# Kernel tuning notes

Hardware: AMD Instinct MI355X
Metric: run time of the kernel (lower is better)

## Reference

```python
import jax, jax.numpy as jnp
import numpy as np

L, H, NH, HD, F, B, S = 32, 1024, 16, 64, 2048, 2, 2048
HPH = H // NH  # hidden per attention head (hyena column split)
EPS = 1e-6
BLOCK = {0:'HCS',4:'HCS',7:'HCS',11:'HCS',14:'HCS',18:'HCS',21:'HCS',25:'HCS',28:'HCS',
         1:'HCM',5:'HCM',8:'HCM',12:'HCM',15:'HCM',19:'HCM',22:'HCM',26:'HCM',29:'HCM',
         2:'HCL',6:'HCL',9:'HCL',13:'HCL',16:'HCL',20:'HCL',23:'HCL',27:'HCL',30:'HCL',
         3:'ATT',10:'ATT',17:'ATT',24:'ATT',31:'ATT'}

def rmsnorm(x, w):
    return x * jax.lax.rsqrt(jnp.mean(x * x, -1, keepdims=True) + EPS) * w

def step_fir(u, state, w, b, flip=False, gated=False):
    # u:[B,C]  state:[B,C,cache]  w:[C,Lf]  b:[C]  (single-token FIR step)
    cache = state.shape[-1]
    w = w[:, ::-1][:, -(cache + 1):] if flip else w[:, :cache + 1]
    y = w[:, -1] * u + jnp.sum(state * w[:, :-1], -1)
    y = y + (b * u if gated else b)
    return y

def split3(z):
    # column_split_hyena=True path of _interleave_split
    r = z.reshape(z.shape[0], NH, 3 * HPH)
    x2 = r[:, :, :HPH].reshape(z.shape[0], H)
    x1 = r[:, :, HPH:2 * HPH].reshape(z.shape[0], H)
    v = r[:, :, 2 * HPH:].reshape(z.shape[0], H)
    return x2, x1, v

def mlp(x, W1, W2):
    return jax.nn.gelu(x @ W1.T) @ W2.T

def fir_block(x, n1, n2, pW, pb, oW, ob, W1, W2, sfw, sfb, h, D, fstate, istate, flip, gated):
    xn = rmsnorm(x, n1)
    z = xn @ pW.T + pb                 # [B,1,3H]
    u = z[:, -1]                       # [B,3H]
    zp = step_fir(u, fstate, sfw, sfb)
    x2, x1, v = split3(zp)
    y = step_fir(x1 * v, istate, h, D, flip=flip, gated=gated)
    y = (y * x2)[:, None]              # [B,1,H]
    x = y @ oW.T + ob + x
    return mlp(rmsnorm(x, n2), W1, W2) + x

def hcl_block(x, n1, n2, pW, pb, oW, ob, W1, W2, sfw, sfb, log_poles, residues, D, fstate, iir):
    xn = rmsnorm(x, n1)
    z = xn @ pW.T + pb
    u = z[:, -1]
    zp = step_fir(u, fstate, sfw, sfb)
    x2, x1, v = split3(zp)
    x1v = x1 * v
    iir_new = jnp.exp(log_poles) * iir + x1v[..., None]   # [B,H,SS] single-step IIR update
    res = jnp.sum(residues * iir_new, -1)
    y = (x2 * (res + D * x1v))[:, None]
    x = y @ oW.T + ob + x
    return mlp(rmsnorm(x, n2), W1, W2) + x

def att_block(x, n1, n2, qW, qb, oW, ob, W1, W2, kc, vc, cos, sin, pos):
    xn = rmsnorm(x, n1)
    qkv = (xn @ qW.T + qb).reshape(B, 1, 3, NH, HD)
    q, k, v = qkv[:, :, 0], qkv[:, :, 1], qkv[:, :, 2]
    c = jnp.concatenate([cos[pos], cos[pos]])  # [HD]
    s = jnp.concatenate([sin[pos], sin[pos]])
    rot = lambda t: jnp.concatenate([-t[..., HD // 2:], t[..., :HD // 2]], -1)
    q = q * c + rot(q) * s
    k = k * c + rot(k) * s
    kc = kc.at[:, pos].set(k[:, 0])  # KV-cache scatter write at current position
    vc = vc.at[:, pos].set(v[:, 0])
    scores = jnp.einsum('bohd,bshd->bhos', q, kc) * (HD ** -0.5)
    scores = jnp.where(jnp.arange(S) > pos, -10000.0, scores)
    aw = jax.nn.softmax(scores, -1)
    ctx = jnp.einsum('bhos,bshd->bohd', aw, vc).reshape(B, 1, H)
    x = ctx @ oW.T + ob + x
    return mlp(rmsnorm(x, n2), W1, W2) + x

def forward(x, position, norm1_w, norm2_w, proj_W, proj_b, out_W, out_b, mlp_W1, mlp_W2,
            sf_w, sf_b, hcs_h, hcs_D, hcm_h, hcm_D, hcl_logpoles, hcl_residues, hcl_D,
            fir_state, hcs_state, hcm_state, iir_state, k_cache, v_cache, rope_cos, rope_sin):
    att = 0
    for i in range(L):  # loop over 32 structurally distinct layers (static)
        t = BLOCK[i]
        cm = (norm1_w[i], norm2_w[i], proj_W[i], proj_b[i], out_W[i], out_b[i], mlp_W1[i], mlp_W2[i])
        if t == 'HCS':
            x = fir_block(x, *cm, sf_w[i], sf_b[i], hcs_h[i], hcs_D[i], fir_state[i], hcs_state[i], False, False)
        elif t == 'HCM':
            x = fir_block(x, *cm, sf_w[i], sf_b[i], hcm_h[i], hcm_D[i], fir_state[i], hcm_state[i], True, True)
        elif t == 'HCL':
            x = hcl_block(x, *cm, sf_w[i], sf_b[i], hcl_logpoles[i], hcl_residues[i], hcl_D[i], fir_state[i], iir_state[i])
        else:
            x = att_block(x, *cm, k_cache[att], v_cache[att], rope_cos, rope_sin, position)
            att += 1
    return x

def setup_inputs():
    key = jax.random.key(0)
    ks = jax.random.split(key, 24)
    g = lambda k, shape, sc: jax.random.normal(k, shape, jnp.float32) * sc
    inv_freq = 1.0 / (10000.0 ** (np.arange(0, HD, 2, dtype=np.float32) / HD))
    ang = np.arange(S, dtype=np.float32)[:, None] * inv_freq[None, :]
    return {
        'x': g(ks[0], (B, 1, H), 1.0),
        'position': 1024,
        'norm1_w': jnp.ones((L, H), jnp.float32),
        'norm2_w': jnp.ones((L, H), jnp.float32),
        'proj_W': g(ks[1], (L, 3 * H, H), H ** -0.5),
        'proj_b': jnp.zeros((L, 3 * H), jnp.float32),
        'out_W': g(ks[2], (L, H, H), 0.2 * H ** -0.5),
        'out_b': jnp.zeros((L, H), jnp.float32),
        'mlp_W1': g(ks[3], (L, F, H), H ** -0.5),
        'mlp_W2': g(ks[4], (L, H, F), 0.2 * F ** -0.5),
        'sf_w': g(ks[5], (L, 3 * H, 3), 0.4),
        'sf_b': g(ks[6], (L, 3 * H), 0.02),
        'hcs_h': g(ks[7], (L, H, 7), 0.2),
        'hcs_D': g(ks[8], (L, H), 0.2),
        'hcm_h': g(ks[9], (L, H, 128), 0.04),
        'hcm_D': g(ks[10], (L, H), 0.2),
        'hcl_logpoles': -jax.random.uniform(ks[11], (L, H, 16), jnp.float32, 0.01, 2.0),
        'hcl_residues': g(ks[12], (L, H, 16), 0.1),
        'hcl_D': g(ks[13], (L, H), 0.2),
        'fir_state': g(ks[14], (L, B, 3 * H, 2), 0.5),
        'hcs_state': g(ks[15], (L, B, H, 6), 0.5),
        'hcm_state': g(ks[16], (L, B, H, 127), 0.5),
        'iir_state': g(ks[17], (L, B, H, 16), 0.5),
        'k_cache': g(ks[18], (5, B, S, NH, HD), 1.0),
        'v_cache': g(ks[19], (5, B, S, NH, HD), 1.0),
        'rope_cos': jnp.asarray(np.cos(ang)),
        'rope_sin': jnp.asarray(np.sin(ang)),
    }

def reference(x, position, norm1_w, norm2_w, proj_W, proj_b, out_W, out_b, mlp_W1, mlp_W2,
              sf_w, sf_b, hcs_h, hcs_D, hcm_h, hcm_D, hcl_logpoles, hcl_residues, hcl_D,
              fir_state, hcs_state, hcm_state, iir_state, k_cache, v_cache, rope_cos, rope_sin):
    return forward(x, position, norm1_w, norm2_w, proj_W, proj_b, out_W, out_b, mlp_W1, mlp_W2,
                   sf_w, sf_b, hcs_h, hcs_D, hcm_h, hcm_D, hcl_logpoles, hcl_residues, hcl_D,
                   fir_state, hcs_state, hcm_state, iir_state, k_cache, v_cache, rope_cos, rope_sin)
```

## Files before the change

kernel.cpp:

```cpp
#include <hip/hip_runtime.h>
#include <hip/hip_bf16.h>
#include <math.h>

#define LAYERS 32
#define H      1024
#define H3     3072
#define NHEADS 16
#define HDIM   64
#define FF     2048
#define BATCH  2
#define SEQ    2048
#define EPSF   1e-6f

__device__ __forceinline__ float wredSum(float v) {
#pragma unroll
  for (int m = 32; m >= 1; m >>= 1) v += __shfl_xor(v, m, 64);
  return v;
}
__device__ __forceinline__ float wredMax(float v) {
#pragma unroll
  for (int m = 32; m >= 1; m >>= 1) v = fmaxf(v, __shfl_xor(v, m, 64));
  return v;
}
__device__ __forceinline__ float gelu_t(float x) {
  return 0.5f * x * (1.0f + tanhf(0.7978845608028654f * (x + 0.044715f * x * x * x)));
}
__device__ __forceinline__ float dot4(float4 a, float4 b) {
  return a.x * b.x + a.y * b.y + a.z * b.z + a.w * b.w;
}

__global__ __launch_bounds__(256) void prep_kernel(
    const float* __restrict__ sf_w, const float* __restrict__ sf_b,
    const float* __restrict__ fir_state,
    const float* __restrict__ hcs_h, const float* __restrict__ hcs_D, const float* __restrict__ hcs_state,
    const float* __restrict__ hcm_h, const float* __restrict__ hcm_D, const float* __restrict__ hcm_state,
    const float* __restrict__ lp, const float* __restrict__ resd, const float* __restrict__ hcl_D,
    const float* __restrict__ iir,
    unsigned long long kbits,
    float* __restrict__ sfd, float* __restrict__ sfc,
    float* __restrict__ mix0, float* __restrict__ mix1)
{
  int blk = blockIdx.x, tid = threadIdx.x;
  if (blk < 768) {
    int idx = blk * 256 + tid;
    int i = idx / (BATCH * H3);
    int r = idx % (BATCH * H3);
    int b = r / H3, ch = r % H3;
    const float* fs = fir_state + ((size_t)(i * BATCH + b) * H3 + ch) * 2;
    const float* sw = sf_w + ((size_t)i * H3 + ch) * 3;
    sfd[idx] = fs[0] * sw[0] + fs[1] * sw[1] + sf_b[i * H3 + ch];
    if (b == 0) sfc[i * H3 + ch] = sw[2];
  } else if (blk < 1024) {
    int idx = (blk - 768) * 256 + tid;
    int i = idx >> 11;
    int r = idx & 2047;
    int b = r >> 10, c = r & 1023;
    int kind = (int)((kbits >> (2 * i)) & 3ull);
    if (kind == 0) {
      const float* st = hcs_state + ((size_t)(i * BATCH + b) * H + c) * 6;
      const float* hh = hcs_h + ((size_t)i * H + c) * 7;
      float acc = 0.f;
#pragma unroll
      for (int k = 0; k < 6; k++) acc += st[k] * hh[k];
      mix0[idx] = acc + hcs_D[i * H + c];
      if (b == 0) mix1[i * H + c] = hh[6];
    } else if (kind == 2) {
      const float* ii = iir + ((size_t)(i * BATCH + b) * H + c) * 16;
      const float* lpp = lp + ((size_t)i * H + c) * 16;
      const float* rs = resd + ((size_t)i * H + c) * 16;
      float acc = 0.f, rsum = 0.f;
#pragma unroll
      for (int k = 0; k < 16; k++) { float rv = rs[k]; acc += rv * expf(lpp[k]) * ii[k]; rsum += rv; }
      mix0[idx] = acc;
      if (b == 0) mix1[i * H + c] = rsum + hcl_D[i * H + c];
    }
  } else {
    int w = tid >> 6, lane = tid & 63;
    int widx = (blk - 1024) * 4 + w;
    if (widx < 9 * BATCH * H) {
      int li = widx >> 11;
      int r = widx & 2047;
      int b = r >> 10, c = r & 1023;
      int i = (li >> 1) * 7 + ((li & 1) ? 5 : 1);
      const float* st = hcm_state + ((size_t)(i * BATCH + b) * H + c) * 127;
      const float* hh = hcm_h + ((size_t)i * H + c) * 128;
      float acc = 0.f;
      int k = lane;
      if (k < 127) acc += st[k] * hh[127 - k];
      k = lane + 64;
      if (k < 127) acc += st[k] * hh[127 - k];
      acc = wredSum(acc);
      if (lane == 0) {
        mix0[(i * BATCH + b) * H + c] = acc;
        if (b == 0) mix1[i * H + c] = hh[0] + hcm_D[i * H + c];
      }
    }
  }
}

template<int ROWS, bool GELU, bool HASBIAS>
__global__ __launch_bounds__(256) void gemv_norm(
    const float* __restrict__ x, const float* __restrict__ nw,
    const float* __restrict__ W, const float* __restrict__ bias,
    float* __restrict__ out)
{
  __shared__ alignas(16) float xe[BATCH * H];
  __shared__ float red[8];
  int tid = threadIdx.x, lane = tid & 63, w = tid >> 6;

  float4 xv0 = ((const float4*)x)[tid];
  float4 xv1 = ((const float4*)x)[tid + 256];
  float4 nv  = ((const float4*)nw)[tid];
  int r = blockIdx.x * 4 + w;
  const float4* rowp = (const float4*)(W + (size_t)r * H);
  float4 wv0 = rowp[lane], wv1 = rowp[lane + 64],
         wv2 = rowp[lane + 128], wv3 = rowp[lane + 192];

  float ss0 = dot4(xv0, xv0), ss1 = dot4(xv1, xv1);
  ((float4*)xe)[tid]       = make_float4(xv0.x * nv.x, xv0.y * nv.y, xv0.z * nv.z, xv0.w * nv.w);
  ((float4*)xe)[tid + 256] = make_float4(xv1.x * nv.x, xv1.y * nv.y, xv1.z * nv.z, xv1.w * nv.w);
  ss0 = wredSum(ss0); ss1 = wredSum(ss1);
  if (lane == 0) { red[w] = ss0; red[4 + w] = ss1; }
  __syncthreads();
  float s0 = rsqrtf((red[0] + red[1] + red[2] + red[3]) * (1.0f / H) + EPSF);
  float s1 = rsqrtf((red[4] + red[5] + red[6] + red[7]) * (1.0f / H) + EPSF);

  const float4* x4 = (const float4*)xe;
  float a0 = dot4(wv0, x4[lane])       + dot4(wv1, x4[lane + 64])
           + dot4(wv2, x4[lane + 128]) + dot4(wv3, x4[lane + 192]);
  float a1 = dot4(wv0, x4[lane + 256]) + dot4(wv1, x4[lane + 320])
           + dot4(wv2, x4[lane + 384]) + dot4(wv3, x4[lane + 448]);
  a0 = wredSum(a0); a1 = wredSum(a1);
  if (lane == 0) {
    float b0 = HASBIAS ? bias[r] : 0.f;
    float v0 = a0 * s0 + b0, v1 = a1 * s1 + b0;
    if (GELU) { v0 = gelu_t(v0); v1 = gelu_t(v1); }
    out[r] = v0;
    out[ROWS + r] = v1;
  }
}

__global__ __launch_bounds__(256) void mix_out_kernel(
    int kind,
    const float* __restrict__ z, const float* __restrict__ sfdL, const float* __restrict__ sfcL,
    const float* __restrict__ mix0L, const float* __restrict__ mix1L,
    const float* __restrict__ attP,
    const float* __restrict__ oW, const float* __restrict__ ob,
    const float* __restrict__ x_in, float* __restrict__ x_out)
{
  __shared__ alignas(16) float ys[BATCH * H];
  int tid = threadIdx.x, lane = tid & 63, w = tid >> 6;
  int r = blockIdx.x * 4 + w;

  if (kind < 3) {
    float x2v[8], x1v[8], vvv[8];
#pragma unroll
    for (int it = 0; it < 8; it++) {
      int e = tid + it * 256;
      int b = e >> 10, c = e & 1023;
      int n = c >> 6, d = c & 63;
      int base = n * 192 + d;
      x2v[it] = sfcL[base] * z[b * H3 + base] + sfdL[b * H3 + base];
      x1v[it] = sfcL[base + 64] * z[b * H3 + base + 64] + sfdL[b * H3 + base + 64];
      vvv[it] = sfcL[base + 128] * z[b * H3 + base + 128] + sfdL[b * H3 + base + 128];
    }
    const float4* rowp = (const float4*)(oW + (size_t)r * H);
    float4 wv0 = rowp[lane], wv1 = rowp[lane + 64],
           wv2 = rowp[lane + 128], wv3 = rowp[lane + 192];
#pragma unroll
    for (int it = 0; it < 8; it++) {
      int e = tid + it * 256;
      int b = e >> 10, c = e & 1023;
      float t = x1v[it] * vvv[it];
      ys[e] = (mix1L[c] * t + mix0L[b * H + c]) * x2v[it];
    }
    __syncthreads();
    const float4* y4 = (const float4*)ys;
    float a0 = dot4(wv0, y4[lane])       + dot4(wv1, y4[lane + 64])
             + dot4(wv2, y4[lane + 128]) + dot4(wv3, y4[lane + 192]);
    float a1 = dot4(wv0, y4[lane + 256]) + dot4(wv1, y4[lane + 320])
             + dot4(wv2, y4[lane + 384]) + dot4(wv3, y4[lane + 448]);
    a0 = wredSum(a0); a1 = wredSum(a1);
    if (lane == 0) {
      x_out[r]     = a0 + ob[r] + x_in[r];
      x_out[H + r] = a1 + ob[r] + x_in[H + r];
    }
  } else {
    const float4* rowp = (const float4*)(oW + (size_t)r * H);
    float4 wv0 = rowp[lane], wv1 = rowp[lane + 64],
           wv2 = rowp[lane + 128], wv3 = rowp[lane + 192];
#pragma unroll
    for (int it = 0; it < 8; it++) {
      int e = tid + it * 256;
      int b = e >> 10, c = e & 1023;
      int n = c >> 6, d = c & 63;
      float M = -1e30f;
#pragma unroll
      for (int sp = 0; sp < 8; sp++) M = fmaxf(M, attP[((sp * BATCH + b) * NHEADS + n) * 66 + 64]);
      float Ls = 0.f, num = 0.f;
#pragma unroll
      for (int sp = 0; sp < 8; sp++) {
        const float* P = attP + ((sp * BATCH + b) * NHEADS + n) * 66;
        float wgt = expf(P[64] - M);
        Ls += wgt * P[65];
        num += wgt * P[d];
      }
      ys[e] = num / Ls;
    }
    __syncthreads();
    const float4* y4 = (const float4*)ys;
    float a0 = dot4(wv0, y4[lane])       + dot4(wv1, y4[lane + 64])
             + dot4(wv2, y4[lane + 128]) + dot4(wv3, y4[lane + 192]);
    float a1 = dot4(wv0, y4[lane + 256]) + dot4(wv1, y4[lane + 320])
             + dot4(wv2, y4[lane + 384]) + dot4(wv3, y4[lane + 448]);
    a0 = wredSum(a0); a1 = wredSum(a1);
    if (lane == 0) {
      x_out[r]     = a0 + ob[r] + x_in[r];
      x_out[H + r] = a1 + ob[r] + x_in[H + r];
    }
  }
}

__global__ __launch_bounds__(256) void gemv_mlp2(
    const float* __restrict__ h, const float* __restrict__ W2,
    const float* __restrict__ xM, float* __restrict__ x_out)
{
  __shared__ alignas(16) float hs[BATCH * FF];
  int tid = threadIdx.x, lane = tid & 63, w = tid >> 6;
  float4 h0 = ((const float4*)h)[tid];
  float4 h1 = ((const float4*)h)[tid + 256];
  float4 h2 = ((const float4*)h)[tid + 512];
  float4 h3 = ((const float4*)h)[tid + 768];
  int r = blockIdx.x * 4 + w;
  const float4* rowp = (const float4*)(W2 + (size_t)r * FF);
  float4 wv[8];
#pragma unroll
  for (int j = 0; j < 8; j++) wv[j] = rowp[lane + 64 * j];

  ((float4*)hs)[tid]       = h0;
  ((float4*)hs)[tid + 256] = h1;
  ((float4*)hs)[tid + 512] = h2;
  ((float4*)hs)[tid + 768] = h3;
  __syncthreads();

  const float4* h4 = (const float4*)hs;
  float a0 = 0.f, a1 = 0.f;
#pragma unroll
  for (int j = 0; j < 8; j++) {
    a0 += dot4(wv[j], h4[lane + 64 * j]);
    a1 += dot4(wv[j], h4[lane + 64 * j + 512]);
  }
  a0 = wredSum(a0); a1 = wredSum(a1);
  if (lane == 0) {
    x_out[r]     = a0 + xM[r];
    x_out[H + r] = a1 + xM[H + r];
  }
}

__global__ __launch_bounds__(256) void attn_kernel(
    const float* __restrict__ z, const int* __restrict__ posp,
    const float* __restrict__ kc, const float* __restrict__ vc,
    const float* __restrict__ cosT, const float* __restrict__ sinT,
    float* __restrict__ P)
{
  int sp = blockIdx.x & 7, n = (blockIdx.x >> 3) & 15, b = blockIdx.x >> 7;
  int pos = *posp;
  __shared__ alignas(16) float q_s[HDIM], k_s[HDIM], v_s[HDIM];
  __shared__ float eg[256];
  __shared__ float redA[4];
  __shared__ alignas(16) float osum[4][HDIM];
  int tid = threadIdx.x, lane = tid & 63, w = tid >> 6;

  if (tid < 64) {
    int d = tid, j = d & 31;
    float cs = cosT[pos * 32 + j], sn = sinT[pos * 32 + j];
    float qv = z[b * H3 + n * 64 + d];
    float qo = z[b * H3 + n * 64 + ((d + 32) & 63)];
    q_s[d] = ((d < 32) ? (qv * cs - qo * sn) : (qv * cs + qo * sn)) * 0.125f;
    float kv = z[b * H3 + 1024 + n * 64 + d];
    float ko = z[b * H3 + 1024 + n * 64 + ((d + 32) & 63)];
    k_s[d] = (d < 32) ? (kv * cs - ko * sn) : (kv * cs + ko * sn);
    v_s[d] = z[b * H3 + 2048 + n * 64 + d];
  }
  __syncthreads();

  int s = sp * 256 + tid;
  float logit = -1e30f;
  if (s <= pos) {
    const float4* k4 = (s == pos) ? (const float4*)k_s
                                  : (const float4*)(kc + (((size_t)b * SEQ + s) * NHEADS + n) * HDIM);
    const float4* q4 = (const float4*)q_s;
    float acc = 0.f;
#pragma unroll
    for (int j = 0; j < 16; j++) acc += dot4(k4[j], q4[j]);
    logit = acc;
  }
  float m = wredMax(logit);
  if (lane == 0) redA[w] = m;
  __syncthreads();
  m = fmaxf(fmaxf(redA[0], redA[1]), fmaxf(redA[2], redA[3]));
  float e = (s <= pos) ? expf(logit - m) : 0.f;
  eg[tid] = e;
  float ps = wredSum(e);
  __syncthreads();
  if (lane == 0) redA[w] = ps;
  __syncthreads();
  float lsum = redA[0] + redA[1] + redA[2] + redA[3];

  int dgrp = lane & 15, srow = lane >> 4;
  float4 acc = make_float4(0.f, 0.f, 0.f, 0.f);
#pragma unroll 4
  for (int it = 0; it < 16; it++) {
    int sl = w * 64 + it * 4;
    if (sp * 256 + sl > pos) break;
    int sli = sl + srow;
    int ss = sp * 256 + sli;
    float ev = eg[sli];
    const float4* v4 = (ss == pos) ? (const float4*)v_s
                                   : (const float4*)(vc + (((size_t)b * SEQ + ss) * NHEADS + n) * HDIM);
    float4 vv = v4[dgrp];
    acc.x += ev * vv.x; acc.y += ev * vv.y; acc.z += ev * vv.z; acc.w += ev * vv.w;
  }
#pragma unroll
  for (int mm = 16; mm <= 32; mm <<= 1) {
    acc.x += __shfl_xor(acc.x, mm, 64);
    acc.y += __shfl_xor(acc.y, mm, 64);
    acc.z += __shfl_xor(acc.z, mm, 64);
    acc.w += __shfl_xor(acc.w, mm, 64);
  }
  if (srow == 0) ((float4*)osum[w])[dgrp] = acc;
  __syncthreads();
  float* Pp = P + ((size_t)(sp * BATCH + b) * NHEADS + n) * 66;
  if (tid < 64) Pp[tid] = osum[0][tid] + osum[1][tid] + osum[2][tid] + osum[3][tid];
  if (tid == 64) Pp[64] = m;
  if (tid == 65) Pp[65] = lsum;
}

extern "C" void kernel_launch(void* const* d_in, const int* in_sizes, int n_in,
                              void* d_out, int out_size, void* d_ws, size_t ws_size,
                              hipStream_t stream) {
  (void)in_sizes; (void)n_in; (void)out_size; (void)ws_size;
  const float* x0    = (const float*)d_in[0];
  const int*   posp  = (const int*)d_in[1];
  const float* n1    = (const float*)d_in[2];
  const float* n2    = (const float*)d_in[3];
  const float* pW    = (const float*)d_in[4];
  const float* pb    = (const float*)d_in[5];
  const float* oW    = (const float*)d_in[6];
  const float* ob    = (const float*)d_in[7];
  const float* W1    = (const float*)d_in[8];
  const float* W2    = (const float*)d_in[9];
  const float* sfw   = (const float*)d_in[10];
  const float* sfb   = (const float*)d_in[11];
  const float* hcs_h = (const float*)d_in[12];
  const float* hcs_D = (const float*)d_in[13];
  const float* hcm_h = (const float*)d_in[14];
  const float* hcm_D = (const float*)d_in[15];
  const float* lp    = (const float*)d_in[16];
  const float* resd  = (const float*)d_in[17];
  const float* hclD  = (const float*)d_in[18];
  const float* fir   = (const float*)d_in[19];
  const float* hcsS  = (const float*)d_in[20];
  const float* hcmS  = (const float*)d_in[21];
  const float* iir   = (const float*)d_in[22];
  const float* kc    = (const float*)d_in[23];
  const float* vc    = (const float*)d_in[24];
  const float* cosT  = (const float*)d_in[25];
  const float* sinT  = (const float*)d_in[26];

  float* ws    = (float*)d_ws;
  float* xbuf0 = ws;
  float* xbuf1 = ws + 2048;
  float* xM    = ws + 4096;
  float* zbuf  = ws + 6144;
  float* hbuf  = ws + 12288;
  float* attP  = ws + 16384;
  float* sfd   = ws + 33280;
  float* sfc   = ws + 229888;
  float* mix0  = ws + 328192;
  float* mix1  = ws + 393728;

  static const int KIND[LAYERS] = {0,1,2,3,0,1,2,0,1,2,3,0,1,2,0,1,2,3,0,1,2,0,1,2,3,0,1,2,0,1,2,3};
  unsigned long long kbits = 0ull;
  for (int i = 0; i < LAYERS; i++) kbits |= ((unsigned long long)KIND[i]) << (2 * i);

  prep_kernel<<<5632, 256, 0, stream>>>(sfw, sfb, fir, hcs_h, hcs_D, hcsS,
      hcm_h, hcm_D, hcmS, lp, resd, hclD, iir, kbits, sfd, sfc, mix0, mix1);

  const float* xsrc = x0;
  int att = 0;
  for (int i = 0; i < LAYERS; i++) {
    gemv_norm<H3, false, true><<<H3 / 4, 256, 0, stream>>>(
        xsrc, n1 + i * H, pW + (size_t)i * H3 * H, pb + i * H3, zbuf);
    if (KIND[i] == 3) {
      attn_kernel<<<256, 256, 0, stream>>>(
          zbuf, posp, kc + (size_t)att * BATCH * SEQ * NHEADS * HDIM,
          vc + (size_t)att * BATCH * SEQ * NHEADS * HDIM, cosT, sinT, attP);
      att++;
    }
    mix_out_kernel<<<H / 4, 256, 0, stream>>>(
        KIND[i], zbuf, sfd + (size_t)i * BATCH * H3, sfc + (size_t)i * H3,
        mix0 + (size_t)i * BATCH * H, mix1 + (size_t)i * H, attP,
        oW + (size_t)i * H * H, ob + i * H, xsrc, xM);
    gemv_norm<FF, true, false><<<FF / 4, 256, 0, stream>>>(
        xM, n2 + i * H, W1 + (size_t)i * FF * H, nullptr, hbuf);
    float* xout = (i == LAYERS - 1) ? (float*)d_out : ((i & 1) ? xbuf1 : xbuf0);
    gemv_mlp2<<<H / 4, 256, 0, stream>>>(
        hbuf, W2 + (size_t)i * H * FF, xM, xout);
    xsrc = xout;
  }
}
```

Measured before the change: 681.1 us.

## Prefetch upcoming layer weights and KV cache into L2 via extra blocks

Adds extra thread blocks to each kernel launch that read ahead the weights needed by later kernels (oW and W1 during the projection GEMV, W2 and the next layer's pW during mix_out and MLP1) and the next attention layer's KV cache during MLP2. The reads are summed and discarded, so they serve only to warm the cache. This aims to hide the DRAM latency of the weight-streaming GEMV chain, which is memory bound at batch 2. In exchange it adds redundant memory traffic and competes for bandwidth and CUs with the real work, and it relies on the prefetched data still being resident in L2/MALL when it is used.

```diff
diff --git a/kernel.cpp b/kernel.cpp
--- a/kernel.cpp
+++ b/kernel.cpp
@@ -29,6 +29,20 @@
   return a.x * b.x + a.y * b.y + a.z * b.z + a.w * b.w;
 }
 
+__device__ __forceinline__ void pf_region(const float4* __restrict__ p, long long n4, int chunk) {
+  long long base = (long long)chunk * 4096 + threadIdx.x;
+  float a0 = 0.f, a1 = 0.f, a2 = 0.f, a3 = 0.f;
+#pragma unroll
+  for (int j = 0; j < 16; j++) {
+    long long idx = base + j * 256;
+    if (idx < n4) {
+      float4 v = p[idx];
+      a0 += v.x; a1 += v.y; a2 += v.z; a3 += v.w;
+    }
+  }
+  asm volatile("" :: "v"(a0), "v"(a1), "v"(a2), "v"(a3));
+}
+
 __global__ __launch_bounds__(256) void prep_kernel(
     const float* __restrict__ sf_w, const float* __restrict__ sf_b,
     const float* __restrict__ fir_state,
@@ -38,9 +52,11 @@
     const float* __restrict__ iir,
     unsigned long long kbits,
     float* __restrict__ sfd, float* __restrict__ sfc,
-    float* __restrict__ mix0, float* __restrict__ mix1)
+    float* __restrict__ mix0, float* __restrict__ mix1,
+    const float4* __restrict__ pf0)
 {
   int blk = blockIdx.x, tid = threadIdx.x;
+  if (blk >= 5632) { pf_region(pf0, 786432LL, blk - 5632); return; }
   if (blk < 768) {
     int idx = blk * 256 + tid;
     int i = idx / (BATCH * H3);
@@ -102,11 +118,20 @@
 __global__ __launch_bounds__(256) void gemv_norm(
     const float* __restrict__ x, const float* __restrict__ nw,
     const float* __restrict__ W, const float* __restrict__ bias,
-    float* __restrict__ out)
+    float* __restrict__ out,
+    const float4* __restrict__ pf0, int c0, long long n0,
+    const float4* __restrict__ pf1, int c1, long long n1)
 {
   __shared__ alignas(16) float xe[BATCH * H];
   __shared__ float red[8];
   int tid = threadIdx.x, lane = tid & 63, w = tid >> 6;
+  const int NFUNC = ROWS / 4;
+  if (blockIdx.x >= NFUNC) {
+    int c = blockIdx.x - NFUNC;
+    if (c < c0) pf_region(pf0, n0, c);
+    else pf_region(pf1, n1, c - c0);
+    return;
+  }
 
   float4 xv0 = ((const float4*)x)[tid];
   float4 xv1 = ((const float4*)x)[tid + 256];
@@ -146,10 +171,18 @@
     const float* __restrict__ mix0L, const float* __restrict__ mix1L,
     const float* __restrict__ attP,
     const float* __restrict__ oW, const float* __restrict__ ob,
-    const float* __restrict__ x_in, float* __restrict__ x_out)
+    const float* __restrict__ x_in, float* __restrict__ x_out,
+    const float4* __restrict__ pf0, int c0, long long n0,
+    const float4* __restrict__ pf1, int c1, long long n1)
 {
   __shared__ alignas(16) float ys[BATCH * H];
   int tid = threadIdx.x, lane = tid & 63, w = tid >> 6;
+  if (blockIdx.x >= 256) {
+    int c = blockIdx.x - 256;
+    if (c < c0) pf_region(pf0, n0, c);
+    else pf_region(pf1, n1, c - c0);
+    return;
+  }
   int r = blockIdx.x * 4 + w;
 
   if (kind < 3) {
@@ -223,10 +256,21 @@
 
 __global__ __launch_bounds__(256) void gemv_mlp2(
     const float* __restrict__ h, const float* __restrict__ W2,
-    const float* __restrict__ xM, float* __restrict__ x_out)
+    const float* __restrict__ xM, float* __restrict__ x_out,
+    const float* __restrict__ kvk, const float* __restrict__ kvv,
+    const int* __restrict__ posp)
 {
   __shared__ alignas(16) float hs[BATCH * FF];
   int tid = threadIdx.x, lane = tid & 63, w = tid >> 6;
+  if (blockIdx.x >= 256) {
+    int c = blockIdx.x - 256;
+    int reg = c >> 7, ch = c & 127;
+    const float* base = (reg & 1) ? kvv : kvk;
+    base += (size_t)(reg >> 1) * SEQ * NHEADS * HDIM;
+    long long n4 = ((long long)(posp[0] + 1) * NHEADS * HDIM) >> 2;
+    pf_region((const float4*)base, n4, ch);
+    return;
+  }
   float4 h0 = ((const float4*)h)[tid];
   float4 h1 = ((const float4*)h)[tid + 256];
   float4 h2 = ((const float4*)h)[tid + 512];
@@ -384,29 +428,43 @@
   unsigned long long kbits = 0ull;
   for (int i = 0; i < LAYERS; i++) kbits |= ((unsigned long long)KIND[i]) << (2 * i);
 
-  prep_kernel<<<5632, 256, 0, stream>>>(sfw, sfb, fir, hcs_h, hcs_D, hcsS,
-      hcm_h, hcm_D, hcmS, lp, resd, hclD, iir, kbits, sfd, sfc, mix0, mix1);
+  prep_kernel<<<5632 + 192, 256, 0, stream>>>(sfw, sfb, fir, hcs_h, hcs_D, hcsS,
+      hcm_h, hcm_D, hcmS, lp, resd, hclD, iir, kbits, sfd, sfc, mix0, mix1,
+      (const float4*)pW);
 
   const float* xsrc = x0;
   int att = 0;
   for (int i = 0; i < LAYERS; i++) {
-    gemv_norm<H3, false, true><<<H3 / 4, 256, 0, stream>>>(
-        xsrc, n1 + i * H, pW + (size_t)i * H3 * H, pb + i * H3, zbuf);
+    gemv_norm<H3, false, true><<<768 + 192, 256, 0, stream>>>(
+        xsrc, n1 + i * H, pW + (size_t)i * H3 * H, pb + i * H3, zbuf,
+        (const float4*)(oW + (size_t)i * H * H), 64, 262144LL,
+        (const float4*)(W1 + (size_t)i * FF * H), 128, 524288LL);
     if (KIND[i] == 3) {
       attn_kernel<<<256, 256, 0, stream>>>(
           zbuf, posp, kc + (size_t)att * BATCH * SEQ * NHEADS * HDIM,
           vc + (size_t)att * BATCH * SEQ * NHEADS * HDIM, cosT, sinT, attP);
       att++;
     }
-    mix_out_kernel<<<H / 4, 256, 0, stream>>>(
+    int cmix = (i < 31) ? 96 : 0;
+    mix_out_kernel<<<256 + 128 + cmix, 256, 0, stream>>>(
         KIND[i], zbuf, sfd + (size_t)i * BATCH * H3, sfc + (size_t)i * H3,
         mix0 + (size_t)i * BATCH * H, mix1 + (size_t)i * H, attP,
-        oW + (size_t)i * H * H, ob + i * H, xsrc, xM);
-    gemv_norm<FF, true, false><<<FF / 4, 256, 0, stream>>>(
-        xM, n2 + i * H, W1 + (size_t)i * FF * H, nullptr, hbuf);
+        oW + (size_t)i * H * H, ob + i * H, xsrc, xM,
+        (const float4*)(W2 + (size_t)i * H * FF), 128, 524288LL,
+        (i < 31) ? (const float4*)(pW + (size_t)(i + 1) * H3 * H) : (const float4*)pW,
+        cmix, 393216LL);
+    int cw1 = (i < 31) ? 96 : 0;
+    gemv_norm<FF, true, false><<<512 + cw1, 256, 0, stream>>>(
+        xM, n2 + i * H, W1 + (size_t)i * FF * H, nullptr, hbuf,
+        (i < 31) ? (const float4*)(pW + (size_t)(i + 1) * H3 * H + 1572864) : (const float4*)pW,
+        cw1, 393216LL,
+        (const float4*)pW, 0, 0LL);
+    bool nextAtt = (i < 31) && (KIND[i + 1] == 3);
+    const float* kcn = nextAtt ? (kc + (size_t)att * BATCH * SEQ * NHEADS * HDIM) : kc;
+    const float* vcn = nextAtt ? (vc + (size_t)att * BATCH * SEQ * NHEADS * HDIM) : vc;
     float* xout = (i == LAYERS - 1) ? (float*)d_out : ((i & 1) ? xbuf1 : xbuf0);
-    gemv_mlp2<<<H / 4, 256, 0, stream>>>(
-        hbuf, W2 + (size_t)i * H * FF, xM, xout);
+    gemv_mlp2<<<256 + (nextAtt ? 512 : 0), 256, 0, stream>>>(
+        hbuf, W2 + (size_t)i * H * FF, xM, xout, kcn, vcn, posp);
     xsrc = xout;
   }
 }
```

Result: slower. 1.204 ms (+76.7%).

## Fuse each layer's GEMV stages into one kernel with atomic-counter dataflow sync

Applied to the files above, without the earlier changes.

Replaces the per-layer sequence of separate launches (input projection, attention, output mix, MLP up, MLP down) with a single kernel per layer. Each stage gets its own block range. Each block loads its weight rows before spinning on global atomic counters that track the previous stage's progress. This removes launch gaps and kernel-boundary drains and lets weight streaming for later stages overlap with earlier compute. The barrier counters are zeroed in the prep kernel. It relies on in-order block dispatch and relaxed atomics for forward progress and visibility, which risks deadlock or stale reads if producer blocks are not resident.

```diff
diff --git a/kernel.cpp b/kernel.cpp
--- a/kernel.cpp
+++ b/kernel.cpp
@@ -17,6 +17,11 @@
   for (int m = 32; m >= 1; m >>= 1) v += __shfl_xor(v, m, 64);
   return v;
 }
+__device__ __forceinline__ int iwredSum(int v) {
+#pragma unroll
+  for (int m = 32; m >= 1; m >>= 1) v += __shfl_xor(v, m, 64);
+  return v;
+}
 __device__ __forceinline__ float wredMax(float v) {
 #pragma unroll
   for (int m = 32; m >= 1; m >>= 1) v = fmaxf(v, __shfl_xor(v, m, 64));
@@ -27,6 +32,295 @@
 }
 __device__ __forceinline__ float dot4(float4 a, float4 b) {
   return a.x * b.x + a.y * b.y + a.z * b.z + a.w * b.w;
+}
+
+__device__ __forceinline__ void ast(float* p, float v) {
+  __hip_atomic_store(p, v, __ATOMIC_RELAXED, __HIP_MEMORY_SCOPE_AGENT);
+}
+__device__ __forceinline__ float ald(const float* p) {
+  return __hip_atomic_load(p, __ATOMIC_RELAXED, __HIP_MEMORY_SCOPE_AGENT);
+}
+
+__device__ __forceinline__ void signal_grp(int* grp, int bid) {
+  __syncthreads();
+  if (threadIdx.x == 0)
+    __hip_atomic_fetch_add(&grp[(bid & 63) * 16], 1, __ATOMIC_RELAXED, __HIP_MEMORY_SCOPE_AGENT);
+}
+__device__ __forceinline__ void wait_grp(int* grp, int need) {
+  if (threadIdx.x < 64) {
+    for (;;) {
+      int v = __hip_atomic_load(&grp[threadIdx.x * 16], __ATOMIC_RELAXED, __HIP_MEMORY_SCOPE_AGENT);
+      if (iwredSum(v) >= need) break;
+      __builtin_amdgcn_s_sleep(2);
+    }
+  }
+  __syncthreads();
+  asm volatile("" ::: "memory");
+}
+
+union SH2 {
+  struct { float xe[2048]; float red[8]; } ns;
+  struct { float ys[2048]; float sml[512]; } mx;
+  struct { float hs[4096]; } w2;
+  struct { float q[64]; float k[64]; float v[64]; float eg[256]; float redA[4]; float osum[4][64]; } att;
+};
+
+__global__ __launch_bounds__(256, 6) void layer_k(
+    int kind,
+    const float* __restrict__ xin, float* __restrict__ xout,
+    const float* __restrict__ n1L, const float* __restrict__ n2L,
+    const float* __restrict__ pWL, const float* __restrict__ pbL,
+    const float* __restrict__ oWL, const float* __restrict__ obL,
+    const float* __restrict__ W1L, const float* __restrict__ W2L,
+    const float* __restrict__ sfcL, const float* __restrict__ sfdL,
+    const float* __restrict__ mix0L, const float* __restrict__ mix1L,
+    const float* __restrict__ kcL, const float* __restrict__ vcL,
+    const int* __restrict__ posp,
+    const float* __restrict__ cosT, const float* __restrict__ sinT,
+    float* __restrict__ z, float* __restrict__ attP,
+    float* __restrict__ xM, float* __restrict__ h,
+    int* __restrict__ barL)
+{
+  __shared__ SH2 sh;
+  int bid = blockIdx.x, tid = threadIdx.x, lane = tid & 63, w = tid >> 6;
+  int* cnt0 = barL;
+  int* cnt1 = barL + 1024;
+  int* cnt2 = barL + 2048;
+  int* cnt3 = barL + 3072;
+
+  int mixBase = (kind == 3) ? 1024 : 768;
+  int w1Base  = (kind == 3) ? 1280 : 1024;
+  int w2Base  = w1Base + 512;
+
+  if (bid < 768) {
+    float4 xv0 = ((const float4*)xin)[tid];
+    float4 xv1 = ((const float4*)xin)[tid + 256];
+    float4 nv  = ((const float4*)n1L)[tid];
+    int r = bid * 4 + w;
+    const float4* rowp = (const float4*)(pWL + (size_t)r * H);
+    float4 wv0 = rowp[lane], wv1 = rowp[lane + 64],
+           wv2 = rowp[lane + 128], wv3 = rowp[lane + 192];
+
+    float ss0 = dot4(xv0, xv0), ss1 = dot4(xv1, xv1);
+    ((float4*)sh.ns.xe)[tid]       = make_float4(xv0.x * nv.x, xv0.y * nv.y, xv0.z * nv.z, xv0.w * nv.w);
+    ((float4*)sh.ns.xe)[tid + 256] = make_float4(xv1.x * nv.x, xv1.y * nv.y, xv1.z * nv.z, xv1.w * nv.w);
+    ss0 = wredSum(ss0); ss1 = wredSum(ss1);
+    if (lane == 0) { sh.ns.red[w] = ss0; sh.ns.red[4 + w] = ss1; }
+    __syncthreads();
+    float s0 = rsqrtf((sh.ns.red[0] + sh.ns.red[1] + sh.ns.red[2] + sh.ns.red[3]) * (1.0f / H) + EPSF);
+    float s1 = rsqrtf((sh.ns.red[4] + sh.ns.red[5] + sh.ns.red[6] + sh.ns.red[7]) * (1.0f / H) + EPSF);
+
+    const float4* x4 = (const float4*)sh.ns.xe;
+    float a0 = dot4(wv0, x4[lane])       + dot4(wv1, x4[lane + 64])
+             + dot4(wv2, x4[lane + 128]) + dot4(wv3, x4[lane + 192]);
+    float a1 = dot4(wv0, x4[lane + 256]) + dot4(wv1, x4[lane + 320])
+             + dot4(wv2, x4[lane + 384]) + dot4(wv3, x4[lane + 448]);
+    a0 = wredSum(a0); a1 = wredSum(a1);
+    if (lane == 0) {
+      float b0 = pbL[r];
+      ast(&z[r], a0 * s0 + b0);
+      ast(&z[H3 + r], a1 * s1 + b0);
+    }
+    signal_grp(cnt0, bid);
+
+  } else if (kind == 3 && bid < 1024) {
+    int mb = bid - 768;
+    int sp = mb & 7, n = (mb >> 3) & 15, b = mb >> 7;
+    int pos = *posp;
+    wait_grp(cnt0, 768);
+    if (tid < 64) {
+      int d = tid, j = d & 31;
+      float cs = cosT[pos * 32 + j], sn = sinT[pos * 32 + j];
+      float qv = ald(&z[b * H3 + n * 64 + d]);
+      float qo = ald(&z[b * H3 + n * 64 + ((d + 32) & 63)]);
+      sh.att.q[d] = ((d < 32) ? (qv * cs - qo * sn) : (qv * cs + qo * sn)) * 0.125f;
+      float kv = ald(&z[b * H3 + 1024 + n * 64 + d]);
+      float ko = ald(&z[b * H3 + 1024 + n * 64 + ((d + 32) & 63)]);
+      sh.att.k[d] = (d < 32) ? (kv * cs - ko * sn) : (kv * cs + ko * sn);
+      sh.att.v[d] = ald(&z[b * H3 + 2048 + n * 64 + d]);
+    }
+    __syncthreads();
+    int s = sp * 256 + tid;
+    float logit = -1e30f;
+    if (s <= pos) {
+      const float4* k4 = (s == pos) ? (const float4*)sh.att.k
+                                    : (const float4*)(kcL + (((size_t)b * SEQ + s) * NHEADS + n) * HDIM);
+      const float4* q4 = (const float4*)sh.att.q;
+      float acc = 0.f;
+#pragma unroll
+      for (int j = 0; j < 16; j++) acc += dot4(k4[j], q4[j]);
+      logit = acc;
+    }
+    float m = wredMax(logit);
+    if (lane == 0) sh.att.redA[w] = m;
+    __syncthreads();
+    m = fmaxf(fmaxf(sh.att.redA[0], sh.att.redA[1]), fmaxf(sh.att.redA[2], sh.att.redA[3]));
+    float e = (s <= pos) ? expf(logit - m) : 0.f;
+    sh.att.eg[tid] = e;
+    float ps = wredSum(e);
+    __syncthreads();
+    if (lane == 0) sh.att.redA[w] = ps;
+    __syncthreads();
+    float lsum = sh.att.redA[0] + sh.att.redA[1] + sh.att.redA[2] + sh.att.redA[3];
+
+    int dgrp = lane & 15, srow = lane >> 4;
+    float4 acc = make_float4(0.f, 0.f, 0.f, 0.f);
+#pragma unroll 4
+    for (int it = 0; it < 16; it++) {
+      int sl = w * 64 + it * 4;
+      if (sp * 256 + sl > pos) break;
+      int sli = sl + srow;
+      int ss2 = sp * 256 + sli;
+      float ev = sh.att.eg[sli];
+      const float4* v4 = (ss2 == pos) ? (const float4*)sh.att.v
+                                      : (const float4*)(vcL + (((size_t)b * SEQ + ss2) * NHEADS + n) * HDIM);
+      float4 vv = v4[dgrp];
+      acc.x += ev * vv.x; acc.y += ev * vv.y; acc.z += ev * vv.z; acc.w += ev * vv.w;
+    }
+#pragma unroll
+    for (int mm = 16; mm <= 32; mm <<= 1) {
+      acc.x += __shfl_xor(acc.x, mm, 64);
+      acc.y += __shfl_xor(acc.y, mm, 64);
+      acc.z += __shfl_xor(acc.z, mm, 64);
+      acc.w += __shfl_xor(acc.w, mm, 64);
+    }
+    if (srow == 0) ((float4*)sh.att.osum[w])[dgrp] = acc;
+    __syncthreads();
+    float* Pp = attP + (size_t)((sp * BATCH + b) * NHEADS + n) * 66;
+    if (tid < 64) ast(&Pp[tid], sh.att.osum[0][tid] + sh.att.osum[1][tid] + sh.att.osum[2][tid] + sh.att.osum[3][tid]);
+    if (tid == 64) ast(&Pp[64], m);
+    if (tid == 65) ast(&Pp[65], lsum);
+    signal_grp(cnt1, bid);
+
+  } else if (bid < w1Base) {
+    int mb = bid - mixBase;
+    int r = mb * 4 + w;
+    const float4* rowp = (const float4*)(oWL + (size_t)r * H);
+    float4 wv0 = rowp[lane], wv1 = rowp[lane + 64],
+           wv2 = rowp[lane + 128], wv3 = rowp[lane + 192];
+
+    if (kind != 3) {
+      wait_grp(cnt0, 768);
+#pragma unroll
+      for (int it = 0; it < 8; it++) {
+        int e = tid + it * 256;
+        int b = e >> 10, c = e & 1023;
+        int n = c >> 6, d = c & 63;
+        int base = n * 192 + d;
+        float z0 = ald(&z[b * H3 + base]);
+        float z1 = ald(&z[b * H3 + base + 64]);
+        float z2 = ald(&z[b * H3 + base + 128]);
+        float x2 = sfcL[base] * z0 + sfdL[b * H3 + base];
+        float x1 = sfcL[base + 64] * z1 + sfdL[b * H3 + base + 64];
+        float vv = sfcL[base + 128] * z2 + sfdL[b * H3 + base + 128];
+        float t = x1 * vv;
+        sh.mx.ys[e] = (mix1L[c] * t + mix0L[b * H + c]) * x2;
+      }
+    } else {
+      wait_grp(cnt1, 256);
+      if (tid < 256) {
+        int sp = tid & 7, n = (tid >> 3) & 15, b = tid >> 7;
+        const float* Pp = attP + (size_t)((sp * BATCH + b) * NHEADS + n) * 66;
+        sh.mx.sml[tid * 2] = ald(&Pp[64]);
+        sh.mx.sml[tid * 2 + 1] = ald(&Pp[65]);
+      }
+      __syncthreads();
+#pragma unroll
+      for (int it = 0; it < 8; it++) {
+        int e = tid + it * 256;
+        int b = e >> 10, c = e & 1023;
+        int n = c >> 6, d = c & 63;
+        float M = -1e30f;
+#pragma unroll
+        for (int sp = 0; sp < 8; sp++) M = fmaxf(M, sh.mx.sml[(((b << 4) | n) * 8 + sp) * 2]);
+        float Ls = 0.f, num = 0.f;
+#pragma unroll
+        for (int sp = 0; sp < 8; sp++) {
+          float Msp = sh.mx.sml[(((b << 4) | n) * 8 + sp) * 2];
+          float Lsp = sh.mx.sml[(((b << 4) | n) * 8 + sp) * 2 + 1];
+          float wgt = expf(Msp - M);
+          Ls += wgt * Lsp;
+          num += wgt * ald(&attP[(size_t)((sp * BATCH + b) * NHEADS + n) * 66 + d]);
+        }
+        sh.mx.ys[e] = num / Ls;
+      }
+    }
+    __syncthreads();
+    const float4* y4 = (const float4*)sh.mx.ys;
+    float a0 = dot4(wv0, y4[lane])       + dot4(wv1, y4[lane + 64])
+             + dot4(wv2, y4[lane + 128]) + dot4(wv3, y4[lane + 192]);
+    float a1 = dot4(wv0, y4[lane + 256]) + dot4(wv1, y4[lane + 320])
+             + dot4(wv2, y4[lane + 384]) + dot4(wv3, y4[lane + 448]);
+    a0 = wredSum(a0); a1 = wredSum(a1);
+    if (lane == 0) {
+      ast(&xM[r],     a0 + obL[r] + xin[r]);
+      ast(&xM[H + r], a1 + obL[r] + xin[H + r]);
+    }
+    signal_grp(cnt2, bid);
+
+  } else if (bid < w2Base) {
+    int wb = bid - w1Base;
+    int r = wb * 4 + w;
+    const float4* rowp = (const float4*)(W1L + (size_t)r * H);
+    float4 wv0 = rowp[lane], wv1 = rowp[lane + 64],
+           wv2 = rowp[lane + 128], wv3 = rowp[lane + 192];
+    wait_grp(cnt2, 256);
+
+    float ss0 = 0.f, ss1 = 0.f;
+#pragma unroll
+    for (int j = 0; j < 4; j++) {
+      float v0 = ald(&xM[4 * tid + j]);
+      float v1 = ald(&xM[1024 + 4 * tid + j]);
+      ss0 += v0 * v0; ss1 += v1 * v1;
+      float nvj = n2L[(4 * tid + j) & 1023];
+      sh.ns.xe[4 * tid + j] = v0 * nvj;
+      sh.ns.xe[1024 + 4 * tid + j] = v1 * nvj;
+    }
+    ss0 = wredSum(ss0); ss1 = wredSum(ss1);
+    if (lane == 0) { sh.ns.red[w] = ss0; sh.ns.red[4 + w] = ss1; }
+    __syncthreads();
+    float s0 = rsqrtf((sh.ns.red[0] + sh.ns.red[1] + sh.ns.red[2] + sh.ns.red[3]) * (1.0f / H) + EPSF);
+    float s1 = rsqrtf((sh.ns.red[4] + sh.ns.red[5] + sh.ns.red[6] + sh.ns.red[7]) * (1.0f / H) + EPSF);
+
+    const float4* x4 = (const float4*)sh.ns.xe;
+    float a0 = dot4(wv0, x4[lane])       + dot4(wv1, x4[lane + 64])
+             + dot4(wv2, x4[lane + 128]) + dot4(wv3, x4[lane + 192]);
+    float a1 = dot4(wv0, x4[lane + 256]) + dot4(wv1, x4[lane + 320])
+             + dot4(wv2, x4[lane + 384]) + dot4(wv3, x4[lane + 448]);
+    a0 = wredSum(a0); a1 = wredSum(a1);
+    if (lane == 0) {
+      ast(&h[r],      gelu_t(a0 * s0));
+      ast(&h[FF + r], gelu_t(a1 * s1));
+    }
+    signal_grp(cnt3, bid);
+
+  } else {
+    int vb = bid - w2Base;
+    int r = vb * 4 + w;
+    const float4* rowp = (const float4*)(W2L + (size_t)r * FF);
+    float4 wv[8];
+#pragma unroll
+    for (int j = 0; j < 8; j++) wv[j] = rowp[lane + 64 * j];
+    wait_grp(cnt3, 512);
+#pragma unroll
+    for (int it = 0; it < 16; it++) {
+      int e = tid + it * 256;
+      sh.w2.hs[e] = ald(&h[e]);
+    }
+    __syncthreads();
+    const float4* h4 = (const float4*)sh.w2.hs;
+    float a0 = 0.f, a1 = 0.f;
+#pragma unroll
+    for (int j = 0; j < 8; j++) {
+      a0 += dot4(wv[j], h4[lane + 64 * j]);
+      a1 += dot4(wv[j], h4[lane + 64 * j + 512]);
+    }
+    a0 = wredSum(a0); a1 = wredSum(a1);
+    if (lane == 0) {
+      xout[r]     = a0 + ald(&xM[r]);
+      xout[H + r] = a1 + ald(&xM[H + r]);
+    }
+  }
 }
 
 __global__ __launch_bounds__(256) void prep_kernel(
@@ -38,7 +332,7 @@
     const float* __restrict__ iir,
     unsigned long long kbits,
     float* __restrict__ sfd, float* __restrict__ sfc,
-    float* __restrict__ mix0, float* __restrict__ mix1)
+    float* __restrict__ mix0, float* __restrict__ mix1, int* __restrict__ bar)
 {
   int blk = blockIdx.x, tid = threadIdx.x;
   if (blk < 768) {
@@ -74,7 +368,7 @@
       mix0[idx] = acc;
       if (b == 0) mix1[i * H + c] = rsum + hcl_D[i * H + c];
     }
-  } else {
+  } else if (blk < 5632) {
     int w = tid >> 6, lane = tid & 63;
     int widx = (blk - 1024) * 4 + w;
     if (widx < 9 * BATCH * H) {
@@ -95,245 +389,10 @@
         if (b == 0) mix1[i * H + c] = hh[0] + hcm_D[i * H + c];
       }
     }
+  } else {
+    int idx = (blk - 5632) * 256 + tid;
+    if (idx < LAYERS * 4096) bar[idx] = 0;
   }
-}
-
-template<int ROWS, bool GELU, bool HASBIAS>
-__global__ __launch_bounds__(256) void gemv_norm(
-    const float* __restrict__ x, const float* __restrict__ nw,
-    const float* __restrict__ W, const float* __restrict__ bias,
-    float* __restrict__ out)
-{
-  __shared__ alignas(16) float xe[BATCH * H];
-  __shared__ float red[8];
-  int tid = threadIdx.x, lane = tid & 63, w = tid >> 6;
-
-  float4 xv0 = ((const float4*)x)[tid];
-  float4 xv1 = ((const float4*)x)[tid + 256];
-  float4 nv  = ((const float4*)nw)[tid];
-  int r = blockIdx.x * 4 + w;
-  const float4* rowp = (const float4*)(W + (size_t)r * H);
-  float4 wv0 = rowp[lane], wv1 = rowp[lane + 64],
-         wv2 = rowp[lane + 128], wv3 = rowp[lane + 192];
-
-  float ss0 = dot4(xv0, xv0), ss1 = dot4(xv1, xv1);
-  ((float4*)xe)[tid]       = make_float4(xv0.x * nv.x, xv0.y * nv.y, xv0.z * nv.z, xv0.w * nv.w);
-  ((float4*)xe)[tid + 256] = make_float4(xv1.x * nv.x, xv1.y * nv.y, xv1.z * nv.z, xv1.w * nv.w);
-  ss0 = wredSum(ss0); ss1 = wredSum(ss1);
-  if (lane == 0) { red[w] = ss0; red[4 + w] = ss1; }
-  __syncthreads();
-  float s0 = rsqrtf((red[0] + red[1] + red[2] + red[3]) * (1.0f / H) + EPSF);
-  float s1 = rsqrtf((red[4] + red[5] + red[6] + red[7]) * (1.0f / H) + EPSF);
-
-  const float4* x4 = (const float4*)xe;
-  float a0 = dot4(wv0, x4[lane])       + dot4(wv1, x4[lane + 64])
-           + dot4(wv2, x4[lane + 128]) + dot4(wv3, x4[lane + 192]);
-  float a1 = dot4(wv0, x4[lane + 256]) + dot4(wv1, x4[lane + 320])
-           + dot4(wv2, x4[lane + 384]) + dot4(wv3, x4[lane + 448]);
-  a0 = wredSum(a0); a1 = wredSum(a1);
-  if (lane == 0) {
-    float b0 = HASBIAS ? bias[r] : 0.f;
-    float v0 = a0 * s0 + b0, v1 = a1 * s1 + b0;
-    if (GELU) { v0 = gelu_t(v0); v1 = gelu_t(v1); }
-    out[r] = v0;
-    out[ROWS + r] = v1;
-  }
-}
-
-__global__ __launch_bounds__(256) void mix_out_kernel(
-    int kind,
-    const float* __restrict__ z, const float* __restrict__ sfdL, const float* __restrict__ sfcL,
-    const float* __restrict__ mix0L, const float* __restrict__ mix1L,
-    const float* __restrict__ attP,
-    const float* __restrict__ oW, const float* __restrict__ ob,
-    const float* __restrict__ x_in, float* __restrict__ x_out)
-{
-  __shared__ alignas(16) float ys[BATCH * H];
-  int tid = threadIdx.x, lane = tid & 63, w = tid >> 6;
-  int r = blockIdx.x * 4 + w;
-
-  if (kind < 3) {
-    float x2v[8], x1v[8], vvv[8];
-#pragma unroll
-    for (int it = 0; it < 8; it++) {
-      int e = tid + it * 256;
-      int b = e >> 10, c = e & 1023;
-      int n = c >> 6, d = c & 63;
-      int base = n * 192 + d;
-      x2v[it] = sfcL[base] * z[b * H3 + base] + sfdL[b * H3 + base];
-      x1v[it] = sfcL[base + 64] * z[b * H3 + base + 64] + sfdL[b * H3 + base + 64];
-      vvv[it] = sfcL[base + 128] * z[b * H3 + base + 128] + sfdL[b * H3 + base + 128];
-    }
-    const float4* rowp = (const float4*)(oW + (size_t)r * H);
-    float4 wv0 = rowp[lane], wv1 = rowp[lane + 64],
-           wv2 = rowp[lane + 128], wv3 = rowp[lane + 192];
-#pragma unroll
-    for (int it = 0; it < 8; it++) {
-      int e = tid + it * 256;
-      int b = e >> 10, c = e & 1023;
-      float t = x1v[it] * vvv[it];
-      ys[e] = (mix1L[c] * t + mix0L[b * H + c]) * x2v[it];
-    }
-    __syncthreads();
-    const float4* y4 = (const float4*)ys;
-    float a0 = dot4(wv0, y4[lane])       + dot4(wv1, y4[lane + 64])
-             + dot4(wv2, y4[lane + 128]) + dot4(wv3, y4[lane + 192]);
-    float a1 = dot4(wv0, y4[lane + 256]) + dot4(wv1, y4[lane + 320])
-             + dot4(wv2, y4[lane + 384]) + dot4(wv3, y4[lane + 448]);
-    a0 = wredSum(a0); a1 = wredSum(a1);
-    if (lane == 0) {
-      x_out[r]     = a0 + ob[r] + x_in[r];
-      x_out[H + r] = a1 + ob[r] + x_in[H + r];
-    }
-  } else {
-    const float4* rowp = (const float4*)(oW + (size_t)r * H);
-    float4 wv0 = rowp[lane], wv1 = rowp[lane + 64],
-           wv2 = rowp[lane + 128], wv3 = rowp[lane + 192];
-#pragma unroll
-    for (int it = 0; it < 8; it++) {
-      int e = tid + it * 256;
-      int b = e >> 10, c = e & 1023;
-      int n = c >> 6, d = c & 63;
-      float M = -1e30f;
-#pragma unroll
-      for (int sp = 0; sp < 8; sp++) M = fmaxf(M, attP[((sp * BATCH + b) * NHEADS + n) * 66 + 64]);
-      float Ls = 0.f, num = 0.f;
-#pragma unroll
-      for (int sp = 0; sp < 8; sp++) {
-        const float* P = attP + ((sp * BATCH + b) * NHEADS + n) * 66;
-        float wgt = expf(P[64] - M);
-        Ls += wgt * P[65];
-        num += wgt * P[d];
-      }
-      ys[e] = num / Ls;
-    }
-    __syncthreads();
-    const float4* y4 = (const float4*)ys;
-    float a0 = dot4(wv0, y4[lane])       + dot4(wv1, y4[lane + 64])
-             + dot4(wv2, y4[lane + 128]) + dot4(wv3, y4[lane + 192]);
-    float a1 = dot4(wv0, y4[lane + 256]) + dot4(wv1, y4[lane + 320])
-             + dot4(wv2, y4[lane + 384]) + dot4(wv3, y4[lane + 448]);
-    a0 = wredSum(a0); a1 = wredSum(a1);
-    if (lane == 0) {
-      x_out[r]     = a0 + ob[r] + x_in[r];
-      x_out[H + r] = a1 + ob[r] + x_in[H + r];
-    }
-  }
-}
-
-__global__ __launch_bounds__(256) void gemv_mlp2(
-    const float* __restrict__ h, const float* __restrict__ W2,
-    const float* __restrict__ xM, float* __restrict__ x_out)
-{
-  __shared__ alignas(16) float hs[BATCH * FF];
-  int tid = threadIdx.x, lane = tid & 63, w = tid >> 6;
-  float4 h0 = ((const float4*)h)[tid];
-  float4 h1 = ((const float4*)h)[tid + 256];
-  float4 h2 = ((const float4*)h)[tid + 512];
-  float4 h3 = ((const float4*)h)[tid + 768];
-  int r = blockIdx.x * 4 + w;
-  const float4* rowp = (const float4*)(W2 + (size_t)r * FF);
-  float4 wv[8];
-#pragma unroll
-  for (int j = 0; j < 8; j++) wv[j] = rowp[lane + 64 * j];
-
-  ((float4*)hs)[tid]       = h0;
-  ((float4*)hs)[tid + 256] = h1;
-  ((float4*)hs)[tid + 512] = h2;
-  ((float4*)hs)[tid + 768] = h3;
-  __syncthreads();
-
-  const float4* h4 = (const float4*)hs;
-  float a0 = 0.f, a1 = 0.f;
-#pragma unroll
-  for (int j = 0; j < 8; j++) {
-    a0 += dot4(wv[j], h4[lane + 64 * j]);
-    a1 += dot4(wv[j], h4[lane + 64 * j + 512]);
-  }
-  a0 = wredSum(a0); a1 = wredSum(a1);
-  if (lane == 0) {
-    x_out[r]     = a0 + xM[r];
-    x_out[H + r] = a1 + xM[H + r];
-  }
-}
-
-__global__ __launch_bounds__(256) void attn_kernel(
-    const float* __restrict__ z, const int* __restrict__ posp,
-    const float* __restrict__ kc, const float* __restrict__ vc,
-    const float* __restrict__ cosT, const float* __restrict__ sinT,
-    float* __restrict__ P)
-{
-  int sp = blockIdx.x & 7, n = (blockIdx.x >> 3) & 15, b = blockIdx.x >> 7;
-  int pos = *posp;
-  __shared__ alignas(16) float q_s[HDIM], k_s[HDIM], v_s[HDIM];
-  __shared__ float eg[256];
-  __shared__ float redA[4];
-  __shared__ alignas(16) float osum[4][HDIM];
-  int tid = threadIdx.x, lane = tid & 63, w = tid >> 6;
-
-  if (tid < 64) {
-    int d = tid, j = d & 31;
-    float cs = cosT[pos * 32 + j], sn = sinT[pos * 32 + j];
-    float qv = z[b * H3 + n * 64 + d];
-    float qo = z[b * H3 + n * 64 + ((d + 32) & 63)];
-    q_s[d] = ((d < 32) ? (qv * cs - qo * sn) : (qv * cs + qo * sn)) * 0.125f;
-    float kv = z[b * H3 + 1024 + n * 64 + d];
-    float ko = z[b * H3 + 1024 + n * 64 + ((d + 32) & 63)];
-    k_s[d] = (d < 32) ? (kv * cs - ko * sn) : (kv * cs + ko * sn);
-    v_s[d] = z[b * H3 + 2048 + n * 64 + d];
-  }
-  __syncthreads();
-
-  int s = sp * 256 + tid;
-  float logit = -1e30f;
-  if (s <= pos) {
-    const float4* k4 = (s == pos) ? (const float4*)k_s
-                                  : (const float4*)(kc + (((size_t)b * SEQ + s) * NHEADS + n) * HDIM);
-    const float4* q4 = (const float4*)q_s;
-    float acc = 0.f;
-#pragma unroll
-    for (int j = 0; j < 16; j++) acc += dot4(k4[j], q4[j]);
-    logit = acc;
-  }
-  float m = wredMax(logit);
-  if (lane == 0) redA[w] = m;
-  __syncthreads();
-  m = fmaxf(fmaxf(redA[0], redA[1]), fmaxf(redA[2], redA[3]));
-  float e = (s <= pos) ? expf(logit - m) : 0.f;
-  eg[tid] = e;
-  float ps = wredSum(e);
-  __syncthreads();
-  if (lane == 0) redA[w] = ps;
-  __syncthreads();
-  float lsum = redA[0] + redA[1] + redA[2] + redA[3];
-
-  int dgrp = lane & 15, srow = lane >> 4;
-  float4 acc = make_float4(0.f, 0.f, 0.f, 0.f);
-#pragma unroll 4
-  for (int it = 0; it < 16; it++) {
-    int sl = w * 64 + it * 4;
-    if (sp * 256 + sl > pos) break;
-    int sli = sl + srow;
-    int ss = sp * 256 + sli;
-    float ev = eg[sli];
-    const float4* v4 = (ss == pos) ? (const float4*)v_s
-                                   : (const float4*)(vc + (((size_t)b * SEQ + ss) * NHEADS + n) * HDIM);
-    float4 vv = v4[dgrp];
-    acc.x += ev * vv.x; acc.y += ev * vv.y; acc.z += ev * vv.z; acc.w += ev * vv.w;
-  }
-#pragma unroll
-  for (int mm = 16; mm <= 32; mm <<= 1) {
-    acc.x += __shfl_xor(acc.x, mm, 64);
-    acc.y += __shfl_xor(acc.y, mm, 64);
-    acc.z += __shfl_xor(acc.z, mm, 64);
-    acc.w += __shfl_xor(acc.w, mm, 64);
-  }
-  if (srow == 0) ((float4*)osum[w])[dgrp] = acc;
-  __syncthreads();
-  float* Pp = P + ((size_t)(sp * BATCH + b) * NHEADS + n) * 66;
-  if (tid < 64) Pp[tid] = osum[0][tid] + osum[1][tid] + osum[2][tid] + osum[3][tid];
-  if (tid == 64) Pp[64] = m;
-  if (tid == 65) Pp[65] = lsum;
 }
 
 extern "C" void kernel_launch(void* const* d_in, const int* in_sizes, int n_in,
@@ -379,34 +438,34 @@
   float* sfc   = ws + 229888;
   float* mix0  = ws + 328192;
   float* mix1  = ws + 393728;
+  int*   bar   = (int*)(ws + 426496);
 
   static const int KIND[LAYERS] = {0,1,2,3,0,1,2,0,1,2,3,0,1,2,0,1,2,3,0,1,2,0,1,2,3,0,1,2,0,1,2,3};
   unsigned long long kbits = 0ull;
   for (int i = 0; i < LAYERS; i++) kbits |= ((unsigned long long)KIND[i]) << (2 * i);
 
-  prep_kernel<<<5632, 256, 0, stream>>>(sfw, sfb, fir, hcs_h, hcs_D, hcsS,
-      hcm_h, hcm_D, hcmS, lp, resd, hclD, iir, kbits, sfd, sfc, mix0, mix1);
+  prep_kernel<<<6144, 256, 0, stream>>>(sfw, sfb, fir, hcs_h, hcs_D, hcsS,
+      hcm_h, hcm_D, hcmS, lp, resd, hclD, iir, kbits, sfd, sfc, mix0, mix1, bar);
 
   const float* xsrc = x0;
   int att = 0;
   for (int i = 0; i < LAYERS; i++) {
-    gemv_norm<H3, false, true><<<H3 / 4, 256, 0, stream>>>(
-        xsrc, n1 + i * H, pW + (size_t)i * H3 * H, pb + i * H3, zbuf);
-    if (KIND[i] == 3) {
-      attn_kernel<<<256, 256, 0, stream>>>(
-          zbuf, posp, kc + (size_t)att * BATCH * SEQ * NHEADS * HDIM,
-          vc + (size_t)att * BATCH * SEQ * NHEADS * HDIM, cosT, sinT, attP);
-      att++;
-    }
-    mix_out_kernel<<<H / 4, 256, 0, stream>>>(
-        KIND[i], zbuf, sfd + (size_t)i * BATCH * H3, sfc + (size_t)i * H3,
-        mix0 + (size_t)i * BATCH * H, mix1 + (size_t)i * H, attP,
-        oW + (size_t)i * H * H, ob + i * H, xsrc, xM);
-    gemv_norm<FF, true, false><<<FF / 4, 256, 0, stream>>>(
-        xM, n2 + i * H, W1 + (size_t)i * FF * H, nullptr, hbuf);
+    int kind = KIND[i];
+    int nb = (kind == 3) ? 2048 : 1792;
     float* xout = (i == LAYERS - 1) ? (float*)d_out : ((i & 1) ? xbuf1 : xbuf0);
-    gemv_mlp2<<<H / 4, 256, 0, stream>>>(
-        hbuf, W2 + (size_t)i * H * FF, xM, xout);
+    const float* kcL = (kind == 3) ? kc + (size_t)att * BATCH * SEQ * NHEADS * HDIM : kc;
+    const float* vcL = (kind == 3) ? vc + (size_t)att * BATCH * SEQ * NHEADS * HDIM : vc;
+    layer_k<<<nb, 256, 0, stream>>>(
+        kind, xsrc, xout,
+        n1 + i * H, n2 + i * H,
+        pW + (size_t)i * H3 * H, pb + i * H3,
+        oW + (size_t)i * H * H, ob + i * H,
+        W1 + (size_t)i * FF * H, W2 + (size_t)i * H * FF,
+        sfc + (size_t)i * H3, sfd + (size_t)i * BATCH * H3,
+        mix0 + (size_t)i * BATCH * H, mix1 + (size_t)i * H,
+        kcL, vcL, posp, cosT, sinT,
+        zbuf, attP, xM, hbuf, bar + (size_t)i * 4096);
+    if (kind == 3) att++;
     xsrc = xout;
   }
 }
```

Measured after the change: 1.071 ms. +57.3%, slower.
